# Kernel optimization log

Measured on AMD Instinct MI355X. Metric: run time of the kernel, lower is better.

Reference implementation:

```python
import jax, jax.numpy as jnp
import numpy as np

B, T, D, H = 2, 2048, 1024, 16
HD = D // H  # 64
EPS = 1e-5

def _ln(x, g, b):
    mu = jnp.mean(x, axis=-1, keepdims=True)
    var = jnp.mean(jnp.square(x - mu), axis=-1, keepdims=True)
    return (x - mu) * jax.lax.rsqrt(var + EPS) * g + b

def setup_inputs() -> dict:
    key = jax.random.key(0)
    ks = jax.random.split(key, 12)
    s = 0.02
    return {
        "x":  jax.random.normal(ks[0], (B, T, D), jnp.float32),
        "Wq": jax.random.normal(ks[1], (H, D, HD), jnp.float32) * s,
        "Wk": jax.random.normal(ks[2], (H, D, HD), jnp.float32) * s,
        "Wv": jax.random.normal(ks[3], (H, D, HD), jnp.float32) * s,
        "Wo": jax.random.normal(ks[4], (D, D), jnp.float32) * s,
        "bo": jnp.zeros((D,), jnp.float32),
        "W1": jax.random.normal(ks[5], (D, 4 * D), jnp.float32) * s,
        "b1": jnp.zeros((4 * D,), jnp.float32),
        "W2": jax.random.normal(ks[6], (4 * D, D), jnp.float32) * s,
        "b2": jnp.zeros((D,), jnp.float32),
        "ln1_g": jnp.ones((D,), jnp.float32),
        "ln1_b": jnp.zeros((D,), jnp.float32),
        "ln2_g": jnp.ones((D,), jnp.float32),
        "ln2_b": jnp.zeros((D,), jnp.float32),
    }

def reference(x, Wq, Wk, Wv, Wo, bo, W1, b1, W2, b2, ln1_g, ln1_b, ln2_g, ln2_b):
    b, t, d = x.shape
    # --- self-attention on ln1(x) ---
    h = _ln(x, ln1_g, ln1_b)
    q = jnp.einsum('btd,hde->bhte', h, Wq)  # [B,H,T,hd]
    k = jnp.einsum('btd,hde->bhte', h, Wk)
    v = jnp.einsum('btd,hde->bhte', h, Wv)
    # NOTE: original code scales by C**-0.5 with C = N_EMBED (not head_size)
    wei = jnp.einsum('bhte,bhse->bhts', q, k) * (d ** -0.5)
    causal = jnp.tril(jnp.ones((t, t), bool))
    wei = jnp.where(causal, wei, -jnp.inf)
    att = jax.nn.softmax(wei, axis=-1)
    o = jnp.einsum('bhts,bhse->bhte', att, v)
    o = o.transpose(0, 2, 1, 3).reshape(b, t, d)  # concat heads
    x = x + o @ Wo + bo
    # --- feed-forward on ln2(x) ---
    h2 = _ln(x, ln2_g, ln2_b)
    ff = jax.nn.relu(h2 @ W1 + b1) @ W2 + b2
    return x + ff
```

## Files before the change

### kernel.cpp

```cpp
#include <hip/hip_runtime.h>
#include <stdint.h>

typedef unsigned short u16;
typedef __attribute__((ext_vector_type(8))) short bf16x8;
typedef __attribute__((ext_vector_type(4))) float f32x4;
typedef __attribute__((ext_vector_type(4))) unsigned int u32x4;
typedef __attribute__((ext_vector_type(2))) unsigned int u32x2;
typedef __attribute__((ext_vector_type(4))) unsigned short u16x4;

#define MFMA16(a, b, c) __builtin_amdgcn_mfma_f32_16x16x32_bf16(a, b, c, 0, 0, 0)
#define VMCNT(N) asm volatile("s_waitcnt vmcnt(" #N ")" ::: "memory")
#define LGKM0() asm volatile("s_waitcnt lgkmcnt(0)" ::: "memory")

__device__ __forceinline__ u16 f2bf(float f) {
  union { float f; uint32_t u; } v; v.f = f;
  uint32_t r = v.u + 0x7FFFu + ((v.u >> 16) & 1u);
  return (u16)(r >> 16);
}

__device__ __forceinline__ float bf2f(u16 u) {
  union { uint32_t u; float f; } v; v.u = ((uint32_t)u) << 16;
  return v.f;
}

__device__ __forceinline__ uint32_t cvt_pk_bf16(float a, float b) {
  uint32_t r;
  asm("v_cvt_pk_bf16_f32 %0, %1, %2" : "=v"(r) : "v"(a), "v"(b));
  return r;
}

__device__ __forceinline__ void gload_lds16(const u16* g, u16* l) {
  __builtin_amdgcn_global_load_lds((const __attribute__((address_space(1))) void*)(g),
                                   (__attribute__((address_space(3))) void*)(l), 16, 0, 0);
}

__global__ __launch_bounds__(256) void ln_kernel(const float* __restrict__ x,
                                                 const float* __restrict__ g,
                                                 const float* __restrict__ beta,
                                                 u16* __restrict__ out) {
  int row = blockIdx.x;
  int tid = threadIdx.x;
  float4 v = ((const float4*)(x + (size_t)row * 1024))[tid];
  float s = v.x + v.y + v.z + v.w;
  float ss = v.x * v.x + v.y * v.y + v.z * v.z + v.w * v.w;
#pragma unroll
  for (int m = 1; m < 64; m <<= 1) { s += __shfl_xor(s, m); ss += __shfl_xor(ss, m); }
  __shared__ float red[8];
  int wave = tid >> 6, lane = tid & 63;
  if (lane == 0) { red[wave] = s; red[4 + wave] = ss; }
  __syncthreads();
  s = red[0] + red[1] + red[2] + red[3];
  ss = red[4] + red[5] + red[6] + red[7];
  float mean = s * (1.0f / 1024.0f);
  float var = ss * (1.0f / 1024.0f) - mean * mean;
  float rstd = rsqrtf(var + 1e-5f);
  float4 gv = ((const float4*)g)[tid];
  float4 bv = ((const float4*)beta)[tid];
  u16x4 o;
  o.x = f2bf((v.x - mean) * rstd * gv.x + bv.x);
  o.y = f2bf((v.y - mean) * rstd * gv.y + bv.y);
  o.z = f2bf((v.z - mean) * rstd * gv.z + bv.z);
  o.w = f2bf((v.w - mean) * rstd * gv.w + bv.w);
  *(u16x4*)(out + (size_t)row * 1024 + tid * 4) = o;
}

__global__ __launch_bounds__(256) void combine_ln(const float* __restrict__ x,
                                                  const u16* __restrict__ p,
                                                  const float* __restrict__ bo,
                                                  const float* __restrict__ g,
                                                  const float* __restrict__ beta,
                                                  float* __restrict__ out,
                                                  u16* __restrict__ h2) {
  int row = blockIdx.x;
  int tid = threadIdx.x;
  size_t i = (size_t)row * 1024 + tid * 4;
  float4 v = *(const float4*)(x + i);
  float4 bb = *(const float4*)(bo + tid * 4);
  v.x += bb.x; v.y += bb.y; v.z += bb.z; v.w += bb.w;
#pragma unroll
  for (int z = 0; z < 4; z++) {
    u16x4 pv = *(const u16x4*)(p + (size_t)z * 4096 * 1024 + i);
    v.x += bf2f(pv.x); v.y += bf2f(pv.y); v.z += bf2f(pv.z); v.w += bf2f(pv.w);
  }
  *(float4*)(out + i) = v;
  float s = v.x + v.y + v.z + v.w;
  float ss = v.x * v.x + v.y * v.y + v.z * v.z + v.w * v.w;
#pragma unroll
  for (int m = 1; m < 64; m <<= 1) { s += __shfl_xor(s, m); ss += __shfl_xor(ss, m); }
  __shared__ float red[8];
  int wave = tid >> 6, lane = tid & 63;
  if (lane == 0) { red[wave] = s; red[4 + wave] = ss; }
  __syncthreads();
  s = red[0] + red[1] + red[2] + red[3];
  ss = red[4] + red[5] + red[6] + red[7];
  float mean = s * (1.0f / 1024.0f);
  float var = ss * (1.0f / 1024.0f) - mean * mean;
  float rstd = rsqrtf(var + 1e-5f);
  float4 gv = ((const float4*)g)[tid];
  float4 bv = ((const float4*)beta)[tid];
  u16x4 o;
  o.x = f2bf((v.x - mean) * rstd * gv.x + bv.x);
  o.y = f2bf((v.y - mean) * rstd * gv.y + bv.y);
  o.z = f2bf((v.z - mean) * rstd * gv.z + bv.z);
  o.w = f2bf((v.w - mean) * rstd * gv.w + bv.w);
  *(u16x4*)(h2 + i) = o;
}

__global__ __launch_bounds__(256) void transpose_f32_bf16(const float* __restrict__ in,
                                                          u16* __restrict__ out,
                                                          int K, int N,
                                                          size_t in_bstride, size_t out_bstride) {
  __shared__ float tile[32][33];
  const float* I = in + (size_t)blockIdx.z * in_bstride;
  u16* O = out + (size_t)blockIdx.z * out_bstride;
  int n0 = blockIdx.x * 32, k0 = blockIdx.y * 32;
  int tx = threadIdx.x & 31, ty = threadIdx.x >> 5;
#pragma unroll
  for (int i = 0; i < 4; i++)
    tile[ty + i * 8][tx] = I[(size_t)(k0 + ty + i * 8) * N + n0 + tx];
  __syncthreads();
#pragma unroll
  for (int i = 0; i < 4; i++)
    O[(size_t)(n0 + ty + i * 8) * K + k0 + tx] = f2bf(tile[tx][ty + i * 8]);
}

template <int EP>
__global__ __launch_bounds__(512, 2) void gemm8p(const u16* __restrict__ A,
                                                 const u16* __restrict__ Bt,
                                                 int M, int N, int K, int KS,
                                                 void* __restrict__ out0,
                                                 u16* __restrict__ out1,
                                                 u16* __restrict__ out2,
                                                 const float* __restrict__ bias) {
  __shared__ __align__(16) u16 lds[65536];
  const int tid = threadIdx.x;
  const int lane = tid & 63, wave = tid >> 6;
  const int lo = lane & 15, hi = lane >> 4;
  const int wm = wave >> 2, wn = wave & 3;
  int gx = gridDim.x;
  int lin = blockIdx.y * gx + blockIdx.x;
  int nwg = gx * gridDim.y;
  int cpx = nwg >> 3;
  int swz = (lin & 7) * cpx + (lin >> 3);
  int bm0 = (swz / gx) * 256, bn0 = (swz % gx) * 256;
  int kbeg = blockIdx.z * KS;
  int T = KS >> 6;

  int rs_ = tid >> 3, ss_ = (tid & 7) ^ (rs_ & 7);
  const u16* srcA = A + (size_t)(bm0 + rs_) * K + kbeg + ss_ * 8;
  const u16* srcB = Bt + (size_t)(bn0 + rs_) * K + kbeg + ss_ * 8;
  const size_t i1 = (size_t)64 * K;
  const size_t h1 = (size_t)128 * K;
  const int dst0 = wave * 512;
  const int dst1 = 4096 + wave * 512;

  const int rpA = wm * 16 + lo;
  const int rpB = wn * 16 + lo;
  const int sp0 = (hi ^ (lo & 7)) * 8;

  f32x4 acc[8][4] = {};
  bf16x8 a[4][2], b0[2][2], b1[2][2];

  auto stageA = [&](int buf, int h, int koff) {
    const u16* s = srcA + koff + (h ? h1 : 0);
    u16* d = lds + (buf * 2 + h) * 8192;
    gload_lds16(s, d + dst0);
    gload_lds16(s + i1, d + dst1);
  };
  auto stageB = [&](int buf, int h, int koff) {
    const u16* s = srcB + koff + (h ? h1 : 0);
    u16* d = lds + 32768 + (buf * 2 + h) * 8192;
    gload_lds16(s, d + dst0);
    gload_lds16(s + i1, d + dst1);
  };
  auto loadA = [&](int buf, int h) {
    const u16* base = lds + (buf * 2 + h) * 8192 + rpA * 64;
#pragma unroll
    for (int m = 0; m < 4; m++) {
      a[m][0] = *(const bf16x8*)(base + m * 2048 + sp0);
      a[m][1] = *(const bf16x8*)(base + m * 2048 + (sp0 ^ 32));
    }
  };
  auto loadB = [&](bf16x8 (&bb)[2][2], int buf, int g) {
    const u16* base = lds + 32768 + (buf * 2 + g) * 8192 + rpB * 64;
#pragma unroll
    for (int n = 0; n < 2; n++) {
      bb[n][0] = *(const bf16x8*)(base + n * 4096 + sp0);
      bb[n][1] = *(const bf16x8*)(base + n * 4096 + (sp0 ^ 32));
    }
  };
  auto mmac = [&](int mh, int np, bf16x8 (&bb)[2][2]) {
    __builtin_amdgcn_s_setprio(1);
#pragma unroll
    for (int m = 0; m < 4; m++)
#pragma unroll
      for (int n = 0; n < 2; n++) {
        acc[mh + m][np + n] = MFMA16(a[m][0], bb[n][0], acc[mh + m][np + n]);
        acc[mh + m][np + n] = MFMA16(a[m][1], bb[n][1], acc[mh + m][np + n]);
      }
    __builtin_amdgcn_s_setprio(0);
  };

  stageA(0, 0, 0); stageB(0, 0, 0); stageB(0, 1, 0); stageA(0, 1, 0);
  VMCNT(4);
  __builtin_amdgcn_s_barrier();

  for (int t = 0; t < T; ++t) {
    int cur = t & 1, nxt = cur ^ 1;
    bool more = (t + 1 < T);
    int koff = (t + 1) * 64;
    loadA(cur, 0); loadB(b0, cur, 0);
    if (more) stageA(nxt, 0, koff);
    __builtin_amdgcn_s_barrier();
    LGKM0();
    __builtin_amdgcn_sched_barrier(0);
    mmac(0, 0, b0);
    __builtin_amdgcn_s_barrier();
    loadB(b1, cur, 1);
    if (more) { stageB(nxt, 0, koff); VMCNT(6); } else { VMCNT(2); }
    __builtin_amdgcn_s_barrier();
    LGKM0();
    __builtin_amdgcn_sched_barrier(0);
    mmac(0, 2, b1);
    __builtin_amdgcn_s_barrier();
    loadA(cur, 1);
    if (more) { stageB(nxt, 1, koff); VMCNT(6); } else { VMCNT(0); }
    __builtin_amdgcn_s_barrier();
    LGKM0();
    __builtin_amdgcn_sched_barrier(0);
    mmac(4, 0, b0);
    __builtin_amdgcn_s_barrier();
    if (more) { stageA(nxt, 1, koff); VMCNT(4); }
    __builtin_amdgcn_s_barrier();
    mmac(4, 2, b1);
    __builtin_amdgcn_s_barrier();
  }

  const int sec = (EP == 0) ? (bn0 >> 10) : 0;
#pragma unroll
  for (int mt = 0; mt < 8; mt++) {
    int gr0 = bm0 + (mt >> 2) * 128 + (mt & 3) * 32 + wm * 16 + hi * 4;
#pragma unroll
    for (int nt = 0; nt < 4; nt++) {
      int gc = bn0 + (nt >> 1) * 128 + (nt & 1) * 64 + wn * 16 + lo;
      if constexpr (EP == 0) {
        int b_ = gr0 >> 11, t_ = gr0 & 2047;
        int nn = gc & 1023, h_ = nn >> 6, e_ = nn & 63;
        size_t bh = (size_t)(b_ * 16 + h_);
        if (sec == 2) {
          u32x2 w;
          w.x = cvt_pk_bf16(acc[mt][nt][0], acc[mt][nt][1]);
          w.y = cvt_pk_bf16(acc[mt][nt][2], acc[mt][nt][3]);
          *(u32x2*)(out2 + (bh * 64 + e_) * 2048 + t_) = w;
        } else {
          float sc = (sec == 0) ? 0.0450842200f : 1.0f;
          u16* dst = (sec == 0) ? (u16*)out0 : out1;
#pragma unroll
          for (int j = 0; j < 4; j++)
            dst[(bh * 2048 + t_ + j) * 64 + e_] = f2bf(acc[mt][nt][j] * sc);
        }
      } else {
#pragma unroll
        for (int j = 0; j < 4; j++) {
          int gr = gr0 + j;
          float val = acc[mt][nt][j];
          if constexpr (EP == 2) {
            float v = val + bias[gc];
            ((u16*)out0)[(size_t)gr * N + gc] = f2bf(fmaxf(v, 0.0f));
          } else if constexpr (EP == 4) {
            ((u16*)out0)[(size_t)blockIdx.z * M * N + (size_t)gr * N + gc] = f2bf(val);
          }
        }
      }
    }
  }
}

__global__ __launch_bounds__(256) void combine4(float* __restrict__ out,
                                                const float* __restrict__ res,
                                                const u16* __restrict__ p,
                                                const float* __restrict__ bias) {
  size_t i = ((size_t)blockIdx.x * 256 + threadIdx.x) * 4;
  float4 r = *(const float4*)(res + i);
  float4 bb = *(const float4*)(bias + (i & 1023));
  float a0 = r.x + bb.x, a1 = r.y + bb.y, a2 = r.z + bb.z, a3 = r.w + bb.w;
#pragma unroll
  for (int z = 0; z < 4; z++) {
    u16x4 v = *(const u16x4*)(p + (size_t)z * 4096 * 1024 + i);
    a0 += bf2f(v.x); a1 += bf2f(v.y); a2 += bf2f(v.z); a3 += bf2f(v.w);
  }
  float4 o4 = {a0, a1, a2, a3};
  *(float4*)(out + i) = o4;
}

__global__ __launch_bounds__(512, 4) void attn_kernel(const u16* __restrict__ q,
                                                      const u16* __restrict__ k,
                                                      const u16* __restrict__ vt,
                                                      u16* __restrict__ o) {
  __shared__ __align__(16) u16 Ks[2][64 * 64];
  __shared__ __align__(16) u16 Vs[2][64 * 64];
  __shared__ __align__(16) u16 Ps[8][16 * 72];
  int bh = blockIdx.y;
  int pi = blockIdx.x;
  int tid = threadIdx.x, lane = tid & 63, wave = tid >> 6;
  int lo = lane & 15, hi = lane >> 4;
  int grp = wave >> 2;
  int qblk_w = grp ? pi : (31 - pi);
  int qb0 = qblk_w * 64;
  int nkb = 32 - pi;
  const u16* qbase = q + (size_t)bh * 2048 * 64;
  const u16* kbase = k + (size_t)bh * 2048 * 64;
  const u16* vbase = vt + (size_t)bh * 64 * 2048;

  int srow = tid >> 3;
  int ssl = (tid & 7) ^ (srow & 7);
  int kOff = srow * 64 + ssl * 8;
  int vOff = srow * 2048 + ssl * 8;

  int qrow = qb0 + (wave & 3) * 16 + lo;
  bf16x8 qf0 = *(const bf16x8*)(qbase + (size_t)qrow * 64 + hi * 8);
  bf16x8 qf1 = *(const bf16x8*)(qbase + (size_t)qrow * 64 + 32 + hi * 8);

  float l_r = 0.0f;
  f32x4 of[4] = {};
  u16* Pw = Ps[wave];

  auto stage = [&](int b, int kb) {
    gload_lds16(kbase + (size_t)kb * 4096 + kOff, Ks[b] + wave * 512);
    gload_lds16(vbase + kb * 64 + vOff, Vs[b] + wave * 512);
  };

  stage(0, 0);
  __syncthreads();

  for (int kb = 0; kb < nkb; kb++) {
    int cur = kb & 1;
    if (kb + 1 < nkb) stage(cur ^ 1, kb + 1);
    if (kb <= qblk_w) {
      const u16* Kb = Ks[cur];
      const u16* Vb = Vs[cur];
      f32x4 s4[4] = {};
#pragma unroll
      for (int nt = 0; nt < 4; nt++) {
        int r = nt * 16 + lo, rw = r & 7;
        bf16x8 kf0 = *(const bf16x8*)(Kb + r * 64 + ((hi ^ rw) << 3));
        bf16x8 kf1 = *(const bf16x8*)(Kb + r * 64 + (((hi + 4) ^ rw) << 3));
        s4[nt] = MFMA16(kf0, qf0, s4[nt]);
        s4[nt] = MFMA16(kf1, qf1, s4[nt]);
      }
      float rs = 0.0f;
      bool diag = (kb == qblk_w);
#pragma unroll
      for (int nt = 0; nt < 4; nt++) {
        float e0, e1, e2, e3;
        if (diag) {
          int key = kb * 64 + nt * 16 + hi * 4;
          e0 = (key     > qrow) ? 0.0f : __builtin_amdgcn_exp2f(s4[nt][0]);
          e1 = (key + 1 > qrow) ? 0.0f : __builtin_amdgcn_exp2f(s4[nt][1]);
          e2 = (key + 2 > qrow) ? 0.0f : __builtin_amdgcn_exp2f(s4[nt][2]);
          e3 = (key + 3 > qrow) ? 0.0f : __builtin_amdgcn_exp2f(s4[nt][3]);
        } else {
          e0 = __builtin_amdgcn_exp2f(s4[nt][0]);
          e1 = __builtin_amdgcn_exp2f(s4[nt][1]);
          e2 = __builtin_amdgcn_exp2f(s4[nt][2]);
          e3 = __builtin_amdgcn_exp2f(s4[nt][3]);
        }
        rs += (e0 + e1) + (e2 + e3);
        u32x2 w;
        w.x = cvt_pk_bf16(e0, e1);
        w.y = cvt_pk_bf16(e2, e3);
        *(u32x2*)(Pw + lo * 72 + nt * 16 + hi * 4) = w;
      }
      rs += __shfl_xor(rs, 16);
      rs += __shfl_xor(rs, 32);
      l_r += rs;
      bf16x8 pb0 = *(const bf16x8*)(Pw + lo * 72 + hi * 8);
      bf16x8 pb1 = *(const bf16x8*)(Pw + lo * 72 + 32 + hi * 8);
#pragma unroll
      for (int et = 0; et < 4; et++) {
        int e = et * 16 + lo, ew = e & 7;
        bf16x8 v0 = *(const bf16x8*)(Vb + e * 64 + ((hi ^ ew) << 3));
        bf16x8 v1 = *(const bf16x8*)(Vb + e * 64 + (((hi + 4) ^ ew) << 3));
        of[et] = MFMA16(v0, pb0, of[et]);
        of[et] = MFMA16(v1, pb1, of[et]);
      }
    }
    __syncthreads();
  }
  int hh = bh & 15, bb = bh >> 4;
  float inv = 1.0f / l_r;
  size_t obase = ((size_t)(bb * 2048 + qrow)) * 1024 + hh * 64 + hi * 4;
#pragma unroll
  for (int et = 0; et < 4; et++) {
    u32x2 w;
    w.x = cvt_pk_bf16(of[et][0] * inv, of[et][1] * inv);
    w.y = cvt_pk_bf16(of[et][2] * inv, of[et][3] * inv);
    *(u32x2*)(o + obase + et * 16) = w;
  }
}

extern "C" void kernel_launch(void* const* d_in, const int* in_sizes, int n_in,
                              void* d_out, int out_size, void* d_ws, size_t ws_size,
                              hipStream_t stream) {
  const float* x = (const float*)d_in[0];
  const float* Wq = (const float*)d_in[1];
  const float* Wk = (const float*)d_in[2];
  const float* Wv = (const float*)d_in[3];
  const float* Wo = (const float*)d_in[4];
  const float* bo = (const float*)d_in[5];
  const float* W1 = (const float*)d_in[6];
  const float* b1 = (const float*)d_in[7];
  const float* W2 = (const float*)d_in[8];
  const float* b2 = (const float*)d_in[9];
  const float* g1 = (const float*)d_in[10];
  const float* be1 = (const float*)d_in[11];
  const float* g2 = (const float*)d_in[12];
  const float* be2 = (const float*)d_in[13];
  float* out = (float*)d_out;
  char* ws = (char*)d_ws;
  const size_t MB = 1024ull * 1024ull;

  u16* h = (u16*)(ws + 0);
  u16* o = h;
  u16* BtQKV = (u16*)(ws + 8 * MB);
  u16* WoT = BtQKV;
  u16* qb = (u16*)(ws + 14 * MB);
  u16* kb = (u16*)(ws + 22 * MB);
  u16* vtb = (u16*)(ws + 30 * MB);
  u16* h2 = vtb;
  u16* pwo = (u16*)(ws + 14 * MB);
  u16* W1T = (u16*)(ws + 38 * MB);
  u16* W2T = W1T;
  u16* yb = (u16*)(ws + 46 * MB);
  u16* pf2 = (u16*)(ws + 0);

  ln_kernel<<<4096, 256, 0, stream>>>(x, g1, be1, h);
  transpose_f32_bf16<<<dim3(2, 32, 16), 256, 0, stream>>>(Wq, BtQKV, 1024, 64,
                                                          (size_t)1024 * 64, (size_t)64 * 1024);
  transpose_f32_bf16<<<dim3(2, 32, 16), 256, 0, stream>>>(Wk, BtQKV + 1024 * 1024, 1024, 64,
                                                          (size_t)1024 * 64, (size_t)64 * 1024);
  transpose_f32_bf16<<<dim3(2, 32, 16), 256, 0, stream>>>(Wv, BtQKV + 2048 * 1024, 1024, 64,
                                                          (size_t)1024 * 64, (size_t)64 * 1024);
  gemm8p<0><<<dim3(12, 16), 512, 0, stream>>>(h, BtQKV, 4096, 3072, 1024, 1024,
                                              (void*)qb, kb, vtb, nullptr);
  attn_kernel<<<dim3(16, 32), 512, 0, stream>>>(qb, kb, vtb, o);
  transpose_f32_bf16<<<dim3(32, 32, 1), 256, 0, stream>>>(Wo, WoT, 1024, 1024, 0, 0);
  gemm8p<4><<<dim3(4, 16, 4), 512, 0, stream>>>(o, WoT, 4096, 1024, 1024, 256,
                                                (void*)pwo, nullptr, nullptr, nullptr);
  combine_ln<<<4096, 256, 0, stream>>>(x, pwo, bo, g2, be2, out, h2);
  transpose_f32_bf16<<<dim3(128, 32, 1), 256, 0, stream>>>(W1, W1T, 1024, 4096, 0, 0);
  gemm8p<2><<<dim3(16, 16), 512, 0, stream>>>(h2, W1T, 4096, 4096, 1024, 1024,
                                              (void*)yb, nullptr, nullptr, b1);
  transpose_f32_bf16<<<dim3(32, 128, 1), 256, 0, stream>>>(W2, W2T, 4096, 1024, 0, 0);
  gemm8p<4><<<dim3(4, 16, 4), 512, 0, stream>>>(yb, W2T, 4096, 1024, 4096, 1024,
                                                (void*)pf2, nullptr, nullptr, nullptr);
  combine4<<<4096, 256, 0, stream>>>(out, out, pf2, b2);
}
```

Baseline: 223.1 us.

## Split causal attention along the key axis into chunks and merge partials

Replaces the paired-q-block attention scheme (512 threads, two q blocks per CTA) with a split-K layout. Each 256-thread CTA handles one 64-row q block and up to 8 key blocks, giving 80 work units per head. Each CTA writes unnormalized bf16 partial outputs and row sums to workspace, and a new attn_merge kernel sums them, normalizes, and writes the concatenated-head output. The goal is more parallelism and better load balance across CUs, at the cost of an extra kernel launch, partial-result traffic, and an extra bf16 rounding of the partials.

After: 234.3 us. 5.0% more time.

```diff
diff --git a/kernel.cpp b/kernel.cpp
--- a/kernel.cpp
+++ b/kernel.cpp
@@ -293,31 +293,37 @@
   *(float4*)(out + i) = o4;
 }
 
-__global__ __launch_bounds__(512, 4) void attn_kernel(const u16* __restrict__ q,
-                                                      const u16* __restrict__ k,
-                                                      const u16* __restrict__ vt,
-                                                      u16* __restrict__ o) {
+__global__ __launch_bounds__(256) void attn_kernel(const u16* __restrict__ q,
+                                                   const u16* __restrict__ k,
+                                                   const u16* __restrict__ vt,
+                                                   u16* __restrict__ po,
+                                                   float* __restrict__ pl) {
   __shared__ __align__(16) u16 Ks[2][64 * 64];
   __shared__ __align__(16) u16 Vs[2][64 * 64];
-  __shared__ __align__(16) u16 Ps[8][16 * 72];
+  __shared__ __align__(16) u16 Ps[4][16 * 72];
   int bh = blockIdx.y;
-  int pi = blockIdx.x;
+  int u = blockIdx.x;
+  int j, c;
+  if (u < 8)       { j = u; c = 0; }
+  else if (u < 24) { j = 8 + ((u - 8) >> 1); c = (u - 8) & 1; }
+  else if (u < 48) { j = 16 + (u - 24) / 3; c = (u - 24) % 3; }
+  else             { j = 24 + ((u - 48) >> 2); c = (u - 48) & 3; }
+  int kstart = c * 8;
+  int kend = min(kstart + 8, j + 1);
+
   int tid = threadIdx.x, lane = tid & 63, wave = tid >> 6;
   int lo = lane & 15, hi = lane >> 4;
-  int grp = wave >> 2;
-  int qblk_w = grp ? pi : (31 - pi);
-  int qb0 = qblk_w * 64;
-  int nkb = 32 - pi;
   const u16* qbase = q + (size_t)bh * 2048 * 64;
   const u16* kbase = k + (size_t)bh * 2048 * 64;
   const u16* vbase = vt + (size_t)bh * 64 * 2048;
 
-  int srow = tid >> 3;
-  int ssl = (tid & 7) ^ (srow & 7);
-  int kOff = srow * 64 + ssl * 8;
-  int vOff = srow * 2048 + ssl * 8;
-
-  int qrow = qb0 + (wave & 3) * 16 + lo;
+  int c0 = tid, c1 = tid + 256;
+  int row0 = c0 >> 3, row1 = c1 >> 3;
+  int sl0 = (c0 & 7) ^ (row0 & 7), sl1 = (c1 & 7) ^ (row1 & 7);
+  int kOff0 = row0 * 64 + sl0 * 8, kOff1 = row1 * 64 + sl1 * 8;
+  int vOff0 = row0 * 2048 + sl0 * 8, vOff1 = row1 * 2048 + sl1 * 8;
+
+  int qrow = j * 64 + wave * 16 + lo;
   bf16x8 qf0 = *(const bf16x8*)(qbase + (size_t)qrow * 64 + hi * 8);
   bf16x8 qf1 = *(const bf16x8*)(qbase + (size_t)qrow * 64 + 32 + hi * 8);
 
@@ -326,77 +332,103 @@
   u16* Pw = Ps[wave];
 
   auto stage = [&](int b, int kb) {
-    gload_lds16(kbase + (size_t)kb * 4096 + kOff, Ks[b] + wave * 512);
-    gload_lds16(vbase + kb * 64 + vOff, Vs[b] + wave * 512);
-  };
-
-  stage(0, 0);
+    gload_lds16(kbase + (size_t)kb * 4096 + kOff0, Ks[b] + wave * 512);
+    gload_lds16(kbase + (size_t)kb * 4096 + kOff1, Ks[b] + 2048 + wave * 512);
+    gload_lds16(vbase + kb * 64 + vOff0, Vs[b] + wave * 512);
+    gload_lds16(vbase + kb * 64 + vOff1, Vs[b] + 2048 + wave * 512);
+  };
+
+  stage(0, kstart);
   __syncthreads();
 
-  for (int kb = 0; kb < nkb; kb++) {
-    int cur = kb & 1;
-    if (kb + 1 < nkb) stage(cur ^ 1, kb + 1);
-    if (kb <= qblk_w) {
-      const u16* Kb = Ks[cur];
-      const u16* Vb = Vs[cur];
-      f32x4 s4[4] = {};
-#pragma unroll
-      for (int nt = 0; nt < 4; nt++) {
-        int r = nt * 16 + lo, rw = r & 7;
-        bf16x8 kf0 = *(const bf16x8*)(Kb + r * 64 + ((hi ^ rw) << 3));
-        bf16x8 kf1 = *(const bf16x8*)(Kb + r * 64 + (((hi + 4) ^ rw) << 3));
-        s4[nt] = MFMA16(kf0, qf0, s4[nt]);
-        s4[nt] = MFMA16(kf1, qf1, s4[nt]);
+  for (int kb = kstart; kb < kend; kb++) {
+    int cur = (kb - kstart) & 1;
+    if (kb + 1 < kend) stage(cur ^ 1, kb + 1);
+    const u16* Kb = Ks[cur];
+    const u16* Vb = Vs[cur];
+    f32x4 s4[4] = {};
+#pragma unroll
+    for (int nt = 0; nt < 4; nt++) {
+      int r = nt * 16 + lo, rw = r & 7;
+      bf16x8 kf0 = *(const bf16x8*)(Kb + r * 64 + ((hi ^ rw) << 3));
+      bf16x8 kf1 = *(const bf16x8*)(Kb + r * 64 + (((hi + 4) ^ rw) << 3));
+      s4[nt] = MFMA16(kf0, qf0, s4[nt]);
+      s4[nt] = MFMA16(kf1, qf1, s4[nt]);
+    }
+    float rs = 0.0f;
+    bool diag = (kb == j);
+#pragma unroll
+    for (int nt = 0; nt < 4; nt++) {
+      float e0, e1, e2, e3;
+      if (diag) {
+        int key = kb * 64 + nt * 16 + hi * 4;
+        e0 = (key     > qrow) ? 0.0f : __builtin_amdgcn_exp2f(s4[nt][0]);
+        e1 = (key + 1 > qrow) ? 0.0f : __builtin_amdgcn_exp2f(s4[nt][1]);
+        e2 = (key + 2 > qrow) ? 0.0f : __builtin_amdgcn_exp2f(s4[nt][2]);
+        e3 = (key + 3 > qrow) ? 0.0f : __builtin_amdgcn_exp2f(s4[nt][3]);
+      } else {
+        e0 = __builtin_amdgcn_exp2f(s4[nt][0]);
+        e1 = __builtin_amdgcn_exp2f(s4[nt][1]);
+        e2 = __builtin_amdgcn_exp2f(s4[nt][2]);
+        e3 = __builtin_amdgcn_exp2f(s4[nt][3]);
       }
-      float rs = 0.0f;
-      bool diag = (kb == qblk_w);
-#pragma unroll
-      for (int nt = 0; nt < 4; nt++) {
-        float e0, e1, e2, e3;
-        if (diag) {
-          int key = kb * 64 + nt * 16 + hi * 4;
-          e0 = (key     > qrow) ? 0.0f : __builtin_amdgcn_exp2f(s4[nt][0]);
-          e1 = (key + 1 > qrow) ? 0.0f : __builtin_amdgcn_exp2f(s4[nt][1]);
-          e2 = (key + 2 > qrow) ? 0.0f : __builtin_amdgcn_exp2f(s4[nt][2]);
-          e3 = (key + 3 > qrow) ? 0.0f : __builtin_amdgcn_exp2f(s4[nt][3]);
-        } else {
-          e0 = __builtin_amdgcn_exp2f(s4[nt][0]);
-          e1 = __builtin_amdgcn_exp2f(s4[nt][1]);
-          e2 = __builtin_amdgcn_exp2f(s4[nt][2]);
-          e3 = __builtin_amdgcn_exp2f(s4[nt][3]);
-        }
-        rs += (e0 + e1) + (e2 + e3);
-        u32x2 w;
-        w.x = cvt_pk_bf16(e0, e1);
-        w.y = cvt_pk_bf16(e2, e3);
-        *(u32x2*)(Pw + lo * 72 + nt * 16 + hi * 4) = w;
-      }
-      rs += __shfl_xor(rs, 16);
-      rs += __shfl_xor(rs, 32);
-      l_r += rs;
-      bf16x8 pb0 = *(const bf16x8*)(Pw + lo * 72 + hi * 8);
-      bf16x8 pb1 = *(const bf16x8*)(Pw + lo * 72 + 32 + hi * 8);
-#pragma unroll
-      for (int et = 0; et < 4; et++) {
-        int e = et * 16 + lo, ew = e & 7;
-        bf16x8 v0 = *(const bf16x8*)(Vb + e * 64 + ((hi ^ ew) << 3));
-        bf16x8 v1 = *(const bf16x8*)(Vb + e * 64 + (((hi + 4) ^ ew) << 3));
-        of[et] = MFMA16(v0, pb0, of[et]);
-        of[et] = MFMA16(v1, pb1, of[et]);
-      }
+      rs += (e0 + e1) + (e2 + e3);
+      u32x2 w;
+      w.x = cvt_pk_bf16(e0, e1);
+      w.y = cvt_pk_bf16(e2, e3);
+      *(u32x2*)(Pw + lo * 72 + nt * 16 + hi * 4) = w;
+    }
+    rs += __shfl_xor(rs, 16);
+    rs += __shfl_xor(rs, 32);
+    l_r += rs;
+    bf16x8 pb0 = *(const bf16x8*)(Pw + lo * 72 + hi * 8);
+    bf16x8 pb1 = *(const bf16x8*)(Pw + lo * 72 + 32 + hi * 8);
+#pragma unroll
+    for (int et = 0; et < 4; et++) {
+      int e = et * 16 + lo, ew = e & 7;
+      bf16x8 v0 = *(const bf16x8*)(Vb + e * 64 + ((hi ^ ew) << 3));
+      bf16x8 v1 = *(const bf16x8*)(Vb + e * 64 + (((hi + 4) ^ ew) << 3));
+      of[et] = MFMA16(v0, pb0, of[et]);
+      of[et] = MFMA16(v1, pb1, of[et]);
     }
     __syncthreads();
   }
-  int hh = bh & 15, bb = bh >> 4;
-  float inv = 1.0f / l_r;
-  size_t obase = ((size_t)(bb * 2048 + qrow)) * 1024 + hh * 64 + hi * 4;
+
+  size_t pbase = ((size_t)(bh * 32 + j) * 4 + c) * 4096;
+  size_t obase = pbase + (size_t)(wave * 16 + lo) * 64 + hi * 4;
 #pragma unroll
   for (int et = 0; et < 4; et++) {
     u32x2 w;
-    w.x = cvt_pk_bf16(of[et][0] * inv, of[et][1] * inv);
-    w.y = cvt_pk_bf16(of[et][2] * inv, of[et][3] * inv);
-    *(u32x2*)(o + obase + et * 16) = w;
-  }
+    w.x = cvt_pk_bf16(of[et][0], of[et][1]);
+    w.y = cvt_pk_bf16(of[et][2], of[et][3]);
+    *(u32x2*)(po + obase + et * 16) = w;
+  }
+  if (hi == 0) pl[(((size_t)(bh * 32 + j) * 4 + c) << 6) + wave * 16 + lo] = l_r;
+}
+
+__global__ __launch_bounds__(256) void attn_merge(const u16* __restrict__ po,
+                                                  const float* __restrict__ pl,
+                                                  u16* __restrict__ o) {
+  int bh = blockIdx.x >> 7;
+  int t0 = (blockIdx.x & 127) * 16;
+  int tid = threadIdx.x;
+  int tt = tid >> 4, dd = (tid & 15) * 4;
+  int t = t0 + tt;
+  int j = t >> 6, tr = t & 63;
+  int nc = (j >> 3) + 1;
+  size_t pbase = ((size_t)(bh * 32 + j) * 4);
+  float a0 = 0, a1 = 0, a2 = 0, a3 = 0, l = 0;
+  for (int c = 0; c < nc; c++) {
+    u16x4 v = *(const u16x4*)(po + (pbase + c) * 4096 + (size_t)tr * 64 + dd);
+    a0 += bf2f(v.x); a1 += bf2f(v.y); a2 += bf2f(v.z); a3 += bf2f(v.w);
+    l += pl[((pbase + c) << 6) + tr];
+  }
+  float inv = 1.0f / l;
+  int hh = bh & 15, bb = bh >> 4;
+  u32x2 w;
+  w.x = cvt_pk_bf16(a0 * inv, a1 * inv);
+  w.y = cvt_pk_bf16(a2 * inv, a3 * inv);
+  *(u32x2*)(o + ((size_t)(bb * 2048 + t)) * 1024 + hh * 64 + dd) = w;
 }
 
 extern "C" void kernel_launch(void* const* d_in, const int* in_sizes, int n_in,
@@ -428,9 +460,11 @@
   u16* kb = (u16*)(ws + 22 * MB);
   u16* vtb = (u16*)(ws + 30 * MB);
   u16* h2 = vtb;
-  u16* pwo = (u16*)(ws + 14 * MB);
+  u16* po = (u16*)(ws + 38 * MB);
+  float* pl = (float*)(ws + 71 * MB + 512 * 1024);
   u16* W1T = (u16*)(ws + 38 * MB);
   u16* W2T = W1T;
+  u16* pwo = (u16*)(ws + 46 * MB);
   u16* yb = (u16*)(ws + 46 * MB);
   u16* pf2 = (u16*)(ws + 0);
 
@@ -443,7 +477,8 @@
                                                           (size_t)1024 * 64, (size_t)64 * 1024);
   gemm8p<0><<<dim3(12, 16), 512, 0, stream>>>(h, BtQKV, 4096, 3072, 1024, 1024,
                                               (void*)qb, kb, vtb, nullptr);
-  attn_kernel<<<dim3(16, 32), 512, 0, stream>>>(qb, kb, vtb, o);
+  attn_kernel<<<dim3(80, 32), 256, 0, stream>>>(qb, kb, vtb, po, pl);
+  attn_merge<<<4096, 256, 0, stream>>>(po, pl, o);
   transpose_f32_bf16<<<dim3(32, 32, 1), 256, 0, stream>>>(Wo, WoT, 1024, 1024, 0, 0);
   gemm8p<4><<<dim3(4, 16, 4), 512, 0, stream>>>(o, WoT, 4096, 1024, 1024, 256,
                                                 (void*)pwo, nullptr, nullptr, nullptr);
```

## Fuse QKV weight transposes and reorder attention causal work assignment

Applied to the files above, without the earlier changes.

Merges the three per-weight QKV transpose launches into one kernel, removing two launches. The attention kernel now gives each block two adjacent query blocks (2u, 2u+1) and launches the heaviest blocks first, replacing the previous pairing of complementary query blocks. Each block's work is therefore no longer equal, so balance depends on heavy-first scheduling. The Wo partial-sum buffer also moves to a different workspace offset.

New measurement: 228.3 us. 2.3% more time.

```diff
diff --git a/kernel.cpp b/kernel.cpp
--- a/kernel.cpp
+++ b/kernel.cpp
@@ -122,6 +122,26 @@
 #pragma unroll
   for (int i = 0; i < 4; i++)
     O[(size_t)(n0 + ty + i * 8) * K + k0 + tx] = f2bf(tile[tx][ty + i * 8]);
+}
+
+__global__ __launch_bounds__(256) void transpose_qkv3(const float* __restrict__ Wq,
+                                                      const float* __restrict__ Wk,
+                                                      const float* __restrict__ Wv,
+                                                      u16* __restrict__ out) {
+  __shared__ float tile[32][33];
+  int w = blockIdx.z >> 4, head = blockIdx.z & 15;
+  const float* src = (w == 0) ? Wq : (w == 1) ? Wk : Wv;
+  const float* I = src + (size_t)head * 1024 * 64;
+  u16* O = out + (size_t)w * 1024 * 1024 + (size_t)head * 64 * 1024;
+  int n0 = blockIdx.x * 32, k0 = blockIdx.y * 32;
+  int tx = threadIdx.x & 31, ty = threadIdx.x >> 5;
+#pragma unroll
+  for (int i = 0; i < 4; i++)
+    tile[ty + i * 8][tx] = I[(size_t)(k0 + ty + i * 8) * 64 + n0 + tx];
+  __syncthreads();
+#pragma unroll
+  for (int i = 0; i < 4; i++)
+    O[(size_t)(n0 + ty + i * 8) * 1024 + k0 + tx] = f2bf(tile[tx][ty + i * 8]);
 }
 
 template <int EP>
@@ -301,13 +321,13 @@
   __shared__ __align__(16) u16 Vs[2][64 * 64];
   __shared__ __align__(16) u16 Ps[8][16 * 72];
   int bh = blockIdx.y;
-  int pi = blockIdx.x;
+  int u = (gridDim.x - 1) - blockIdx.x;
   int tid = threadIdx.x, lane = tid & 63, wave = tid >> 6;
   int lo = lane & 15, hi = lane >> 4;
   int grp = wave >> 2;
-  int qblk_w = grp ? pi : (31 - pi);
+  int qblk_w = 2 * u + grp;
   int qb0 = qblk_w * 64;
-  int nkb = 32 - pi;
+  int nkb = 2 * u + 2;
   const u16* qbase = q + (size_t)bh * 2048 * 64;
   const u16* kbase = k + (size_t)bh * 2048 * 64;
   const u16* vbase = vt + (size_t)bh * 64 * 2048;
@@ -428,19 +448,14 @@
   u16* kb = (u16*)(ws + 22 * MB);
   u16* vtb = (u16*)(ws + 30 * MB);
   u16* h2 = vtb;
-  u16* pwo = (u16*)(ws + 14 * MB);
   u16* W1T = (u16*)(ws + 38 * MB);
   u16* W2T = W1T;
+  u16* pwo = (u16*)(ws + 46 * MB);
   u16* yb = (u16*)(ws + 46 * MB);
   u16* pf2 = (u16*)(ws + 0);
 
   ln_kernel<<<4096, 256, 0, stream>>>(x, g1, be1, h);
-  transpose_f32_bf16<<<dim3(2, 32, 16), 256, 0, stream>>>(Wq, BtQKV, 1024, 64,
-                                                          (size_t)1024 * 64, (size_t)64 * 1024);
-  transpose_f32_bf16<<<dim3(2, 32, 16), 256, 0, stream>>>(Wk, BtQKV + 1024 * 1024, 1024, 64,
-                                                          (size_t)1024 * 64, (size_t)64 * 1024);
-  transpose_f32_bf16<<<dim3(2, 32, 16), 256, 0, stream>>>(Wv, BtQKV + 2048 * 1024, 1024, 64,
-                                                          (size_t)1024 * 64, (size_t)64 * 1024);
+  transpose_qkv3<<<dim3(2, 32, 48), 256, 0, stream>>>(Wq, Wk, Wv, BtQKV);
   gemm8p<0><<<dim3(12, 16), 512, 0, stream>>>(h, BtQKV, 4096, 3072, 1024, 1024,
                                               (void*)qb, kb, vtb, nullptr);
   attn_kernel<<<dim3(16, 32), 512, 0, stream>>>(qb, kb, vtb, o);
```
